# Kernel optimization log

Hardware: AMD Instinct MI355X
Metric: run time of the kernel (lower is better)

The kernel has to match this reference:

```python
import jax, jax.numpy as jnp
import numpy as np

INPUT_SIZE = 512
NUM_CLASSES = 80
R_MAX = 16           # max gaussian radius given box-size bounds in setup_inputs
EPS32 = 1.1920929e-07  # torch.finfo(torch.float32).eps


def _gaussian_radius(h, w, min_overlap=0.3):
    # vectorized port of gaussian_radius()
    b1 = h + w
    c1 = w * h * (1 - min_overlap) / (1 + min_overlap)
    sq1 = jnp.sqrt(b1 ** 2 - 4 * c1)
    r1 = (b1 - sq1) / 2.0
    b2 = 2 * (h + w)
    c2 = (1 - min_overlap) * w * h
    sq2 = jnp.sqrt(b2 ** 2 - 16 * c2)
    r2 = (b2 - sq2) / 8.0
    a3 = 4 * min_overlap
    b3 = -2 * min_overlap * (h + w)
    c3 = (min_overlap - 1) * w * h
    sq3 = jnp.sqrt(b3 ** 2 - 4 * a3 * c3)
    r3 = (b3 + sq3) / (2 * a3)
    return jnp.minimum(jnp.minimum(r1, r2), r3)


def _build_targets(boxes, labels, B, C, H, W):
    w_ratio = float(W) / INPUT_SIZE
    h_ratio = float(H) / INPUT_SIZE
    cx = (boxes[..., 0] + boxes[..., 2]) * w_ratio / 2.0   # [B,N]
    cy = (boxes[..., 1] + boxes[..., 3]) * h_ratio / 2.0
    cxi = jnp.floor(cx).astype(jnp.int32)
    cyi = jnp.floor(cy).astype(jnp.int32)
    sw = (boxes[..., 2] - boxes[..., 0]) * w_ratio          # scaled box w
    sh = (boxes[..., 3] - boxes[..., 1]) * h_ratio          # scaled box h
    rad = jnp.maximum(0.0, jnp.floor(_gaussian_radius(sh, sw))).astype(jnp.int32)  # [B,N]

    # fixed (2*R_MAX+1)^2 window, masked per-box to the true radius
    offs = jnp.arange(-R_MAX, R_MAX + 1)
    dx = offs[None, :]            # [1,K]
    dy = offs[:, None]            # [K,1]
    dist2 = (dx * dx + dy * dy).astype(jnp.float32)         # [K,K]
    d = (2 * rad + 1).astype(jnp.float32)                   # diameter
    sigma2 = (2.0 * d / 6.0) * (d / 6.0)                    # matches 2*diameter/6*diameter/6
    kern = jnp.exp(-dist2[None, None] / sigma2[..., None, None])  # [B,N,K,K]
    kern = jnp.where(kern < EPS32, 0.0, kern)               # kernel.max()==1
    inwin = (jnp.abs(dx)[None, None] <= rad[..., None, None]) & \
            (jnp.abs(dy)[None, None] <= rad[..., None, None])

    yy = cyi[:, :, None, None] + dy[None, None]             # [B,N,K,1]
    xx = cxi[:, :, None, None] + dx[None, None]             # [B,N,1,K]
    valid = inwin & (yy >= 0) & (yy < H) & (xx >= 0) & (xx < W)
    vals = jnp.where(valid, kern, 0.0)                      # [B,N,K,K]
    bidx = jnp.arange(B)[:, None, None, None]
    lab = labels[:, :, None, None].astype(jnp.int32)
    flat = ((bidx * C + lab) * H + jnp.clip(yy, 0, H - 1)) * W + jnp.clip(xx, 0, W - 1)
    center_true = jnp.zeros(B * C * H * W, jnp.float32).at[flat.reshape(-1)].max(
        vals.reshape(-1)).reshape(B, C, H, W)

    # point scatters for wh / offset / weight (in-bounds by construction)
    pflat = (jnp.arange(B)[:, None] * H + cyi) * W + cxi    # [B,N]
    pf = pflat.ravel()
    wh0 = jnp.zeros(B * H * W, jnp.float32).at[pf].set(sw.ravel()).reshape(B, H, W)
    wh1 = jnp.zeros(B * H * W, jnp.float32).at[pf].set(sh.ravel()).reshape(B, H, W)
    wh_true = jnp.stack([wh0, wh1], axis=1)                 # [B,2,H,W]
    of0 = jnp.zeros(B * H * W, jnp.float32).at[pf].set((cx - cxi).ravel()).reshape(B, H, W)
    of1 = jnp.zeros(B * H * W, jnp.float32).at[pf].set((cy - cyi).ravel()).reshape(B, H, W)
    offset_true = jnp.stack([of0, of1], axis=1)             # [B,2,H,W]
    wmap = jnp.zeros(B * H * W, jnp.float32).at[pf].set(1.0).reshape(B, H, W)
    weight = jnp.broadcast_to(wmap[:, None], (B, 2, H, W))
    avg_factor = jnp.maximum(1.0, (center_true == 1.0).sum().astype(jnp.float32))
    return center_true, wh_true, offset_true, weight, avg_factor


def setup_inputs() -> dict:
    key = jax.random.key(0)
    k1, k2, k3, k4, k5 = jax.random.split(key, 5)
    B, N = 16, 64
    center_pred = jax.random.uniform(k1, (B, NUM_CLASSES, 128, 128), dtype=jnp.float32)
    wh_pred = jax.random.normal(k2, (B, 2, 128, 128), dtype=jnp.float32)
    offset_pred = jax.random.normal(k3, (B, 2, 128, 128), dtype=jnp.float32)
    u = jax.random.uniform(k4, (B, N, 4), dtype=jnp.float32)
    ctr_x = 8.0 + u[..., 0] * 496.0
    ctr_y = 8.0 + u[..., 1] * 496.0
    bw = 16.0 + u[..., 2] * 240.0
    bh = 16.0 + u[..., 3] * 240.0
    boxes = jnp.stack([ctr_x - bw / 2, ctr_y - bh / 2,
                       ctr_x + bw / 2, ctr_y + bh / 2], axis=-1)
    labels = jax.random.randint(k5, (B, N), 0, NUM_CLASSES, dtype=jnp.int32)
    return {"center_pred": center_pred, "wh_pred": wh_pred,
            "offset_pred": offset_pred, "boxes": boxes, "labels": labels}


def reference(center_pred, wh_pred, offset_pred, boxes, labels):
    B, C, H, W = center_pred.shape
    ct, wt, ot, ww, af = _build_targets(boxes, labels, B, C, H, W)
    # GaussianFocalLoss(alpha=2, gamma=4, loss_weight=1)
    pos_w = (ct == 1.0).astype(center_pred.dtype)
    neg_w = (1.0 - ct) ** 4.0
    neg = -jnp.log(1.0 - center_pred + 1e-12) * center_pred ** 2 * neg_w
    pos = -jnp.log(center_pred + 1e-12) * (1.0 - center_pred) ** 2 * pos_w
    loss_center = (pos + neg).sum() / (af + EPS32)
    # L1 losses with weight map, average_factor*2
    loss_wh = 0.1 * (jnp.abs(wh_pred - wt) * ww).sum() / (af * 2.0 + EPS32)
    loss_offset = 1.0 * (jnp.abs(offset_pred - ot) * ww).sum() / (af * 2.0 + EPS32)
    return loss_center + loss_wh + loss_offset
```

## Files before the change

### kernel.cpp

```cpp
#include <hip/hip_runtime.h>
#include <math.h>

#define EPS32 1.1920929e-07f

constexpr int B = 16, C = 80, H = 128, W = 128, NBOX = 64;
constexpr int NCORR = B * NBOX;
constexpr int NSTREAM = 1024;
constexpr int NBLK = NCORR + NSTREAM;
constexpr int NTOT = B * C * H * W;
constexpr int NV4 = NTOT / 4;
constexpr int SSTRIDE = NSTREAM * 256;

__device__ __forceinline__ float f0_term(float p) {
    return -__logf(1.0f - p + 1e-12f) * p * p;
}

__device__ __forceinline__ float block_reduce_add(float v, float* sred) {
    #pragma unroll
    for (int off = 32; off > 0; off >>= 1)
        v += __shfl_down(v, off, 64);
    int lane = threadIdx.x & 63;
    int wid  = threadIdx.x >> 6;
    if (lane == 0) sred[wid] = v;
    __syncthreads();
    if (threadIdx.x == 0) {
        float s = sred[0];
        #pragma unroll
        for (int i = 1; i < 4; ++i) s += sred[i];
        return s;
    }
    return 0.0f;
}

__global__ __launch_bounds__(256) void fused_kernel(
    const float* __restrict__ cp, const float* __restrict__ whp,
    const float* __restrict__ ofp, const float* __restrict__ boxes,
    const int* __restrict__ labels, float4* __restrict__ ws4)
{
    __shared__ float sred[4];
    const int t = threadIdx.x;
    float my_wh = 0.0f, my_of = 0.0f, my_af = 0.0f;
    float center = 0.0f;

    if (blockIdx.x < (unsigned)NCORR) {
        __shared__ int   scx[NBOX], scy[NBOX], sre[NBOX], slab[NBOX], slist[NBOX];
        __shared__ float sinv[NBOX], ssw[NBOX], ssh[NBOX], sox[NBOX], soy[NBOX];
        __shared__ int   nlist;
        const int k = blockIdx.x;
        const int b = k >> 6;
        const int n = k & 63;

        if (t < NBOX) {
            const float* bx = boxes + ((b * NBOX + t) << 2);
            float x1 = bx[0], y1 = bx[1], x2 = bx[2], y2 = bx[3];
            float cx = (x1 + x2) * 0.25f * 0.5f;
            float cy = (y1 + y2) * 0.25f * 0.5f;
            int cxi = (int)floorf(cx);
            int cyi = (int)floorf(cy);
            float sw = (x2 - x1) * 0.25f;
            float sh = (y2 - y1) * 0.25f;
            float h = sh, w = sw;
            float b1 = h + w;
            float c1 = w * h * 0.7f / 1.3f;
            float r1 = (b1 - sqrtf(b1 * b1 - 4.0f * c1)) * 0.5f;
            float b2 = 2.0f * (h + w);
            float c2 = 0.7f * w * h;
            float r2 = (b2 - sqrtf(b2 * b2 - 16.0f * c2)) * 0.125f;
            float b3 = -0.6f * (h + w);
            float c3 = -0.7f * w * h;
            float r3 = (b3 + sqrtf(b3 * b3 - 4.8f * c3)) / 2.4f;
            float r = fminf(fminf(r1, r2), r3);
            int rad = (int)fmaxf(0.0f, floorf(r));
            float d = (float)(2 * rad + 1);
            float sigma2 = 2.0f * d / 6.0f * (d / 6.0f);
            scx[t] = cxi; scy[t] = cyi;
            sre[t] = rad < 16 ? rad : 16;
            slab[t] = labels[b * NBOX + t];
            sinv[t] = 1.0f / sigma2;
            ssw[t] = sw; ssh[t] = sh;
            sox[t] = cx - (float)cxi; soy[t] = cy - (float)cyi;
        }
        __syncthreads();

        if (t == 0) {
            int c = slab[n], L = 0;
            for (int m = 0; m < NBOX; ++m) if (slab[m] == c) slist[L++] = m;
            nlist = L;
            bool winner = true;
            for (int m = n + 1; m < NBOX; ++m)
                if (scx[m] == scx[n] && scy[m] == scy[n]) { winner = false; break; }
            if (winner) {
                int cxi = scx[n], cyi = scy[n];
                int i0 = ((b * 2 + 0) * H + cyi) * W + cxi;
                int i1 = ((b * 2 + 1) * H + cyi) * W + cxi;
                my_wh = fabsf(whp[i0] - ssw[n]) + fabsf(whp[i1] - ssh[n]);
                my_of = fabsf(ofp[i0] - sox[n]) + fabsf(ofp[i1] - soy[n]);
            }
            bool first = true;
            for (int m = 0; m < n; ++m)
                if (slab[m] == slab[n] && scx[m] == scx[n] && scy[m] == scy[n]) { first = false; break; }
            if (first) my_af = 1.0f;
        }
        __syncthreads();

        const int c  = slab[n];
        const int R  = sre[n];
        const int Wd = 2 * R + 1;
        const int cells = Wd * Wd;
        const int cx0 = scx[n], cy0 = scy[n];
        const int L = nlist;
        float corr = 0.0f;
        for (int cell = t; cell < cells; cell += 256) {
            int dy = cell / Wd - R;
            int dx = cell - (dy + R) * Wd - R;
            int y = cy0 + dy, x = cx0 + dx;
            if ((unsigned)y >= (unsigned)H || (unsigned)x >= (unsigned)W) continue;
            int minm = NBOX;
            float ct = 0.0f;
            for (int i = 0; i < L; ++i) {
                int m = slist[i];
                int ddx = x - scx[m], ddy = y - scy[m];
                int re = sre[m];
                if (ddx > re || ddx < -re || ddy > re || ddy < -re) continue;
                if (m < minm) minm = m;
                float d2 = (float)(ddx * ddx + ddy * ddy);
                float kv = (d2 == 0.0f) ? 1.0f : __expf(-d2 * sinv[m]);
                if (kv < EPS32) kv = 0.0f;
                ct = fmaxf(ct, kv);
            }
            if (minm != n) continue;
            float p = cp[((b * C + c) * H + y) * W + x];
            float lt = __logf(1.0f - p + 1e-12f);
            float omc = 1.0f - ct;
            float w2 = omc * omc;
            float w4 = w2 * w2;
            float val = -lt * p * p * (w4 - 1.0f);
            if (ct == 1.0f) {
                float q = 1.0f - p;
                val += -__logf(p + 1e-12f) * q * q;
            }
            corr += val;
        }
        center = block_reduce_add(corr, sred);
    } else {
        const float4* cp4 = (const float4*)cp;
        const int base = (blockIdx.x - NCORR) * 256 + t;
        float s0 = 0.0f, s1 = 0.0f, s2 = 0.0f, s3 = 0.0f;
        #pragma unroll 1
        for (int j = 0; j < 20; j += 4) {
            float4 a = cp4[base + (j + 0) * SSTRIDE];
            float4 b = cp4[base + (j + 1) * SSTRIDE];
            float4 c = cp4[base + (j + 2) * SSTRIDE];
            float4 d = cp4[base + (j + 3) * SSTRIDE];
            s0 += f0_term(a.x) + f0_term(a.y) + f0_term(a.z) + f0_term(a.w);
            s1 += f0_term(b.x) + f0_term(b.y) + f0_term(b.z) + f0_term(b.w);
            s2 += f0_term(c.x) + f0_term(c.y) + f0_term(c.z) + f0_term(c.w);
            s3 += f0_term(d.x) + f0_term(d.y) + f0_term(d.z) + f0_term(d.w);
        }
        center = block_reduce_add((s0 + s1) + (s2 + s3), sred);
    }

    if (t == 0) {
        float4 out;
        out.x = center; out.y = my_wh; out.z = my_of; out.w = my_af;
        ws4[blockIdx.x] = out;
    }
}

__global__ __launch_bounds__(256) void finalize_kernel(
    const float4* __restrict__ ws4, float* __restrict__ out)
{
    __shared__ float sred[4];
    float c = 0.0f, wh = 0.0f, of = 0.0f, af = 0.0f;
    for (int i = threadIdx.x; i < NBLK; i += 256) {
        float4 v = ws4[i];
        c += v.x; wh += v.y; of += v.z; af += v.w;
    }
    float cs = block_reduce_add(c, sred);  __syncthreads();
    float ws = block_reduce_add(wh, sred); __syncthreads();
    float os = block_reduce_add(of, sred); __syncthreads();
    float as = block_reduce_add(af, sred);
    if (threadIdx.x == 0) {
        float a = fmaxf(1.0f, as);
        out[0] = cs / (a + EPS32)
               + 0.1f * ws / (a * 2.0f + EPS32)
               + os / (a * 2.0f + EPS32);
    }
}

extern "C" void kernel_launch(void* const* d_in, const int* in_sizes, int n_in,
                              void* d_out, int out_size, void* d_ws, size_t ws_size,
                              hipStream_t stream) {
    const float* cp     = (const float*)d_in[0];
    const float* whp    = (const float*)d_in[1];
    const float* ofp    = (const float*)d_in[2];
    const float* boxes  = (const float*)d_in[3];
    const int*   labels = (const int*)d_in[4];
    float4* ws4 = (float4*)d_ws;

    fused_kernel<<<NBLK, 256, 0, stream>>>(cp, whp, ofp, boxes, labels, ws4);
    finalize_kernel<<<1, 256, 0, stream>>>(ws4, (float*)d_out);
}
```

Measured before the change: 130.8 us.

## Merge streaming and correction work per block and fuse finalize via cooperative grid sync

The kernel now gives every one of the 1024 blocks both a slice of the dense log-term stream over center_pred and one box's window correction, replacing the previous split between correction blocks and separate streaming blocks. Per-box bookkeeping (same-label candidate list, winner and first-occurrence checks) is computed with wave ballots instead of a serial loop in thread 0. When occupancy allows, the final reduction runs inside the same kernel after a cooperative grid sync, removing the second launch. The aim is better load balance and less launch and serial overhead, at the cost of a grid-wide barrier and a cooperative launch requirement.

```diff
diff --git a/kernel.cpp b/kernel.cpp
--- a/kernel.cpp
+++ b/kernel.cpp
@@ -1,15 +1,18 @@
 #include <hip/hip_runtime.h>
+#include <hip/hip_cooperative_groups.h>
 #include <math.h>
 
+namespace cg = cooperative_groups;
+
 #define EPS32 1.1920929e-07f
 
 constexpr int B = 16, C = 80, H = 128, W = 128, NBOX = 64;
-constexpr int NCORR = B * NBOX;
-constexpr int NSTREAM = 1024;
-constexpr int NBLK = NCORR + NSTREAM;
+constexpr int NBLK = B * NBOX;
 constexpr int NTOT = B * C * H * W;
-constexpr int NV4 = NTOT / 4;
-constexpr int SSTRIDE = NSTREAM * 256;
+constexpr int NV4  = NTOT / 4;
+constexpr int SSTRIDE = NBLK * 256;
+constexpr int SITER = NV4 / SSTRIDE;
+static_assert(SITER * SSTRIDE == NV4, "streaming must tile exactly");
 
 __device__ __forceinline__ float f0_term(float p) {
     return -__logf(1.0f - p + 1e-12f) * p * p;
@@ -32,139 +35,178 @@
     return 0.0f;
 }
 
-__global__ __launch_bounds__(256) void fused_kernel(
+__device__ __forceinline__ float4 block_partial(
+    const float* __restrict__ cp, const float* __restrict__ whp,
+    const float* __restrict__ ofp, const float* __restrict__ boxes,
+    const int* __restrict__ labels, float* sred)
+{
+    __shared__ int   scx[NBOX], scy[NBOX], sre[NBOX], slab[NBOX];
+    __shared__ float sinv[NBOX];
+    __shared__ unsigned long long cand_mask;
+    __shared__ float s_woa[3];
+    const int t = threadIdx.x;
+    const int k = blockIdx.x;
+    const int b = k >> 6;
+    const int n = k & 63;
+
+    float sw_t = 0.0f, sh_t = 0.0f, ox_t = 0.0f, oy_t = 0.0f;
+    if (t < NBOX) {
+        const float* bx = boxes + ((b * NBOX + t) << 2);
+        float x1 = bx[0], y1 = bx[1], x2 = bx[2], y2 = bx[3];
+        float cx = (x1 + x2) * 0.25f * 0.5f;
+        float cy = (y1 + y2) * 0.25f * 0.5f;
+        int cxi = (int)floorf(cx);
+        int cyi = (int)floorf(cy);
+        float sw = (x2 - x1) * 0.25f;
+        float sh = (y2 - y1) * 0.25f;
+        float h = sh, w = sw;
+        float b1 = h + w;
+        float c1 = w * h * 0.7f / 1.3f;
+        float r1 = (b1 - sqrtf(b1 * b1 - 4.0f * c1)) * 0.5f;
+        float b2 = 2.0f * (h + w);
+        float c2 = 0.7f * w * h;
+        float r2 = (b2 - sqrtf(b2 * b2 - 16.0f * c2)) * 0.125f;
+        float b3 = -0.6f * (h + w);
+        float c3 = -0.7f * w * h;
+        float r3 = (b3 + sqrtf(b3 * b3 - 4.8f * c3)) / 2.4f;
+        float r = fminf(fminf(r1, r2), r3);
+        int rad = (int)fmaxf(0.0f, floorf(r));
+        float d = (float)(2 * rad + 1);
+        float sigma2 = 2.0f * d / 6.0f * (d / 6.0f);
+        scx[t] = cxi; scy[t] = cyi;
+        sre[t] = rad < 16 ? rad : 16;
+        slab[t] = labels[b * NBOX + t];
+        sinv[t] = 1.0f / sigma2;
+        sw_t = sw; sh_t = sh;
+        ox_t = cx - (float)cxi; oy_t = cy - (float)cyi;
+        if (t == 0) { s_woa[0] = 0.0f; s_woa[1] = 0.0f; s_woa[2] = 0.0f; }
+    }
+    __syncthreads();
+
+    if (t < NBOX) {
+        const int cxn = scx[n], cyn = scy[n], labn = slab[n];
+        bool same_cell = (scx[t] == cxn) && (scy[t] == cyn);
+        unsigned long long clash = __ballot(same_cell && (t > n));
+        unsigned long long firstm = __ballot(same_cell && (slab[t] == labn) && (t < n));
+        unsigned long long cand = __ballot(slab[t] == labn);
+        if (t == n) {
+            cand_mask = cand;
+            if (clash == 0ULL) {
+                int i0 = ((b * 2 + 0) * H + cyn) * W + cxn;
+                int i1 = ((b * 2 + 1) * H + cyn) * W + cxn;
+                s_woa[0] = fabsf(whp[i0] - sw_t) + fabsf(whp[i1] - sh_t);
+                s_woa[1] = fabsf(ofp[i0] - ox_t) + fabsf(ofp[i1] - oy_t);
+            }
+            if (firstm == 0ULL) s_woa[2] = 1.0f;
+        }
+    }
+
+    const float4* cp4 = (const float4*)cp;
+    const int base = k * 256 + t;
+    float s0 = 0.0f, s1 = 0.0f, s2 = 0.0f, s3 = 0.0f;
+    #pragma unroll 1
+    for (int j = 0; j < SITER; j += 4) {
+        float4 a = cp4[base + (j + 0) * SSTRIDE];
+        float4 bb = cp4[base + (j + 1) * SSTRIDE];
+        float4 c = cp4[base + (j + 2) * SSTRIDE];
+        float4 dd = cp4[base + (j + 3) * SSTRIDE];
+        s0 += f0_term(a.x) + f0_term(a.y) + f0_term(a.z) + f0_term(a.w);
+        s1 += f0_term(bb.x) + f0_term(bb.y) + f0_term(bb.z) + f0_term(bb.w);
+        s2 += f0_term(c.x) + f0_term(c.y) + f0_term(c.z) + f0_term(c.w);
+        s3 += f0_term(dd.x) + f0_term(dd.y) + f0_term(dd.z) + f0_term(dd.w);
+    }
+    float center = (s0 + s1) + (s2 + s3);
+
+    __syncthreads();
+
+    const int c   = slab[n];
+    const int R   = sre[n];
+    const int Wd  = 2 * R + 1;
+    const int cells = Wd * Wd;
+    const int cx0 = scx[n], cy0 = scy[n];
+    const unsigned long long cmask = cand_mask;
+    float corr = 0.0f;
+    for (int cell = t; cell < cells; cell += 256) {
+        int dy = cell / Wd - R;
+        int dx = cell - (dy + R) * Wd - R;
+        int y = cy0 + dy, x = cx0 + dx;
+        if ((unsigned)y >= (unsigned)H || (unsigned)x >= (unsigned)W) continue;
+        int minm = NBOX;
+        float ct = 0.0f;
+        unsigned long long mm = cmask;
+        while (mm) {
+            int m = __ffsll(mm) - 1;
+            mm &= mm - 1;
+            int ddx = x - scx[m], ddy = y - scy[m];
+            int re = sre[m];
+            if (ddx > re || ddx < -re || ddy > re || ddy < -re) continue;
+            if (m < minm) minm = m;
+            float d2 = (float)(ddx * ddx + ddy * ddy);
+            float kv = (d2 == 0.0f) ? 1.0f : __expf(-d2 * sinv[m]);
+            if (kv < EPS32) kv = 0.0f;
+            ct = fmaxf(ct, kv);
+        }
+        if (minm != n) continue;
+        float p = cp[((b * C + c) * H + y) * W + x];
+        float lt = __logf(1.0f - p + 1e-12f);
+        float omc = 1.0f - ct;
+        float w2 = omc * omc;
+        float w4 = w2 * w2;
+        float val = -lt * p * p * (w4 - 1.0f);
+        if (ct == 1.0f) {
+            float q = 1.0f - p;
+            val += -__logf(p + 1e-12f) * q * q;
+        }
+        corr += val;
+    }
+    center += corr;
+
+    float cs = block_reduce_add(center, sred);
+    float4 out4 = {0.0f, 0.0f, 0.0f, 0.0f};
+    if (t == 0) {
+        out4.x = cs;
+        out4.y = s_woa[0]; out4.z = s_woa[1]; out4.w = s_woa[2];
+    }
+    return out4;
+}
+
+__global__ __launch_bounds__(256, 4) void fused_coop(
+    const float* __restrict__ cp, const float* __restrict__ whp,
+    const float* __restrict__ ofp, const float* __restrict__ boxes,
+    const int* __restrict__ labels, float4* __restrict__ ws4,
+    float* __restrict__ out)
+{
+    __shared__ float sred[4];
+    float4 p = block_partial(cp, whp, ofp, boxes, labels, sred);
+    if (threadIdx.x == 0) ws4[blockIdx.x] = p;
+    cg::this_grid().sync();
+    if (blockIdx.x == 0) {
+        float c = 0.0f, wh = 0.0f, of = 0.0f, af = 0.0f;
+        for (int i = threadIdx.x; i < NBLK; i += 256) {
+            float4 v = ws4[i];
+            c += v.x; wh += v.y; of += v.z; af += v.w;
+        }
+        float cs = block_reduce_add(c, sred);  __syncthreads();
+        float ws = block_reduce_add(wh, sred); __syncthreads();
+        float os = block_reduce_add(of, sred); __syncthreads();
+        float as = block_reduce_add(af, sred);
+        if (threadIdx.x == 0) {
+            float a = fmaxf(1.0f, as);
+            out[0] = cs / (a + EPS32)
+                   + 0.1f * ws / (a * 2.0f + EPS32)
+                   + os / (a * 2.0f + EPS32);
+        }
+    }
+}
+
+__global__ __launch_bounds__(256, 4) void fused_plain(
     const float* __restrict__ cp, const float* __restrict__ whp,
     const float* __restrict__ ofp, const float* __restrict__ boxes,
     const int* __restrict__ labels, float4* __restrict__ ws4)
 {
     __shared__ float sred[4];
-    const int t = threadIdx.x;
-    float my_wh = 0.0f, my_of = 0.0f, my_af = 0.0f;
-    float center = 0.0f;
-
-    if (blockIdx.x < (unsigned)NCORR) {
-        __shared__ int   scx[NBOX], scy[NBOX], sre[NBOX], slab[NBOX], slist[NBOX];
-        __shared__ float sinv[NBOX], ssw[NBOX], ssh[NBOX], sox[NBOX], soy[NBOX];
-        __shared__ int   nlist;
-        const int k = blockIdx.x;
-        const int b = k >> 6;
-        const int n = k & 63;
-
-        if (t < NBOX) {
-            const float* bx = boxes + ((b * NBOX + t) << 2);
-            float x1 = bx[0], y1 = bx[1], x2 = bx[2], y2 = bx[3];
-            float cx = (x1 + x2) * 0.25f * 0.5f;
-            float cy = (y1 + y2) * 0.25f * 0.5f;
-            int cxi = (int)floorf(cx);
-            int cyi = (int)floorf(cy);
-            float sw = (x2 - x1) * 0.25f;
-            float sh = (y2 - y1) * 0.25f;
-            float h = sh, w = sw;
-            float b1 = h + w;
-            float c1 = w * h * 0.7f / 1.3f;
-            float r1 = (b1 - sqrtf(b1 * b1 - 4.0f * c1)) * 0.5f;
-            float b2 = 2.0f * (h + w);
-            float c2 = 0.7f * w * h;
-            float r2 = (b2 - sqrtf(b2 * b2 - 16.0f * c2)) * 0.125f;
-            float b3 = -0.6f * (h + w);
-            float c3 = -0.7f * w * h;
-            float r3 = (b3 + sqrtf(b3 * b3 - 4.8f * c3)) / 2.4f;
-            float r = fminf(fminf(r1, r2), r3);
-            int rad = (int)fmaxf(0.0f, floorf(r));
-            float d = (float)(2 * rad + 1);
-            float sigma2 = 2.0f * d / 6.0f * (d / 6.0f);
-            scx[t] = cxi; scy[t] = cyi;
-            sre[t] = rad < 16 ? rad : 16;
-            slab[t] = labels[b * NBOX + t];
-            sinv[t] = 1.0f / sigma2;
-            ssw[t] = sw; ssh[t] = sh;
-            sox[t] = cx - (float)cxi; soy[t] = cy - (float)cyi;
-        }
-        __syncthreads();
-
-        if (t == 0) {
-            int c = slab[n], L = 0;
-            for (int m = 0; m < NBOX; ++m) if (slab[m] == c) slist[L++] = m;
-            nlist = L;
-            bool winner = true;
-            for (int m = n + 1; m < NBOX; ++m)
-                if (scx[m] == scx[n] && scy[m] == scy[n]) { winner = false; break; }
-            if (winner) {
-                int cxi = scx[n], cyi = scy[n];
-                int i0 = ((b * 2 + 0) * H + cyi) * W + cxi;
-                int i1 = ((b * 2 + 1) * H + cyi) * W + cxi;
-                my_wh = fabsf(whp[i0] - ssw[n]) + fabsf(whp[i1] - ssh[n]);
-                my_of = fabsf(ofp[i0] - sox[n]) + fabsf(ofp[i1] - soy[n]);
-            }
-            bool first = true;
-            for (int m = 0; m < n; ++m)
-                if (slab[m] == slab[n] && scx[m] == scx[n] && scy[m] == scy[n]) { first = false; break; }
-            if (first) my_af = 1.0f;
-        }
-        __syncthreads();
-
-        const int c  = slab[n];
-        const int R  = sre[n];
-        const int Wd = 2 * R + 1;
-        const int cells = Wd * Wd;
-        const int cx0 = scx[n], cy0 = scy[n];
-        const int L = nlist;
-        float corr = 0.0f;
-        for (int cell = t; cell < cells; cell += 256) {
-            int dy = cell / Wd - R;
-            int dx = cell - (dy + R) * Wd - R;
-            int y = cy0 + dy, x = cx0 + dx;
-            if ((unsigned)y >= (unsigned)H || (unsigned)x >= (unsigned)W) continue;
-            int minm = NBOX;
-            float ct = 0.0f;
-            for (int i = 0; i < L; ++i) {
-                int m = slist[i];
-                int ddx = x - scx[m], ddy = y - scy[m];
-                int re = sre[m];
-                if (ddx > re || ddx < -re || ddy > re || ddy < -re) continue;
-                if (m < minm) minm = m;
-                float d2 = (float)(ddx * ddx + ddy * ddy);
-                float kv = (d2 == 0.0f) ? 1.0f : __expf(-d2 * sinv[m]);
-                if (kv < EPS32) kv = 0.0f;
-                ct = fmaxf(ct, kv);
-            }
-            if (minm != n) continue;
-            float p = cp[((b * C + c) * H + y) * W + x];
-            float lt = __logf(1.0f - p + 1e-12f);
-            float omc = 1.0f - ct;
-            float w2 = omc * omc;
-            float w4 = w2 * w2;
-            float val = -lt * p * p * (w4 - 1.0f);
-            if (ct == 1.0f) {
-                float q = 1.0f - p;
-                val += -__logf(p + 1e-12f) * q * q;
-            }
-            corr += val;
-        }
-        center = block_reduce_add(corr, sred);
-    } else {
-        const float4* cp4 = (const float4*)cp;
-        const int base = (blockIdx.x - NCORR) * 256 + t;
-        float s0 = 0.0f, s1 = 0.0f, s2 = 0.0f, s3 = 0.0f;
-        #pragma unroll 1
-        for (int j = 0; j < 20; j += 4) {
-            float4 a = cp4[base + (j + 0) * SSTRIDE];
-            float4 b = cp4[base + (j + 1) * SSTRIDE];
-            float4 c = cp4[base + (j + 2) * SSTRIDE];
-            float4 d = cp4[base + (j + 3) * SSTRIDE];
-            s0 += f0_term(a.x) + f0_term(a.y) + f0_term(a.z) + f0_term(a.w);
-            s1 += f0_term(b.x) + f0_term(b.y) + f0_term(b.z) + f0_term(b.w);
-            s2 += f0_term(c.x) + f0_term(c.y) + f0_term(c.z) + f0_term(c.w);
-            s3 += f0_term(d.x) + f0_term(d.y) + f0_term(d.z) + f0_term(d.w);
-        }
-        center = block_reduce_add((s0 + s1) + (s2 + s3), sred);
-    }
-
-    if (t == 0) {
-        float4 out;
-        out.x = center; out.y = my_wh; out.z = my_of; out.w = my_af;
-        ws4[blockIdx.x] = out;
-    }
+    float4 p = block_partial(cp, whp, ofp, boxes, labels, sred);
+    if (threadIdx.x == 0) ws4[blockIdx.x] = p;
 }
 
 __global__ __launch_bounds__(256) void finalize_kernel(
@@ -197,7 +239,23 @@
     const float* boxes  = (const float*)d_in[3];
     const int*   labels = (const int*)d_in[4];
     float4* ws4 = (float4*)d_ws;
-
-    fused_kernel<<<NBLK, 256, 0, stream>>>(cp, whp, ofp, boxes, labels, ws4);
-    finalize_kernel<<<1, 256, 0, stream>>>(ws4, (float*)d_out);
-}
+    float*  outp = (float*)d_out;
+
+    static int coop = -1;
+    if (coop < 0) {
+        int maxb = 0;
+        hipError_t e = hipOccupancyMaxActiveBlocksPerMultiprocessor(
+            &maxb, (const void*)fused_coop, 256, 0);
+        coop = (e == hipSuccess && maxb >= 4) ? 1 : 0;
+    }
+
+    if (coop) {
+        void* args[] = {(void*)&cp, (void*)&whp, (void*)&ofp,
+                        (void*)&boxes, (void*)&labels, (void*)&ws4, (void*)&outp};
+        hipLaunchCooperativeKernel((const void*)fused_coop, dim3(NBLK), dim3(256),
+                                   args, 0, stream);
+    } else {
+        fused_plain<<<NBLK, 256, 0, stream>>>(cp, whp, ofp, boxes, labels, ws4);
+        finalize_kernel<<<1, 256, 0, stream>>>(ws4, outp);
+    }
+}
```

After: 231.9 us. 77.2% more time.
